# Kernel tuning notes

Hardware: AMD Instinct MI355X
Metric: run time of the kernel (lower is better)

The kernel has to match this reference:

```python
import jax, jax.numpy as jnp
import numpy as np

L = 2048
LEVEL = 4
B = 16
D = 32

# pywt 'db4' decomposition filters (dec_lo, dec_hi), hardcoded to avoid pywt dep
DB4_DEC_LO = np.array([
    -0.010597401784997278, 0.032883011666982945, 0.030841381835986965,
    -0.18703481171888114, -0.02798376941698385, 0.6308807679295904,
    0.7148465705525415, 0.23037781330885523])
DB4_DEC_HI = np.array([
    -0.23037781330885523, 0.7148465705525415, -0.6308807679295904,
    -0.02798376941698385, 0.18703481171888114, 0.030841381835986965,
    -0.032883011666982945, -0.010597401784997278])


def _wavelet_dec_filter(vec, length, level):
    # filter[j][t][(t - 2^j * i) mod L] = vec[i]  (vectorized over t, i)
    wl = len(vec)
    f = np.zeros((level, length, length), dtype=np.float32)
    t = np.arange(length)[:, None]
    i = np.arange(wl)[None, :]
    rows = np.broadcast_to(t, (length, wl))
    for j in range(level):
        idx = (t - (2 ** j) * i) % length  # (L, wl)
        f[j, rows, idx] = vec[None, :]
    return f


def setup_inputs() -> dict:
    key = jax.random.key(0)
    x = jax.random.normal(key, (B, L, D), dtype=jnp.float32)
    h = DB4_DEC_HI / np.sqrt(2.0)
    g = DB4_DEC_LO / np.sqrt(2.0)
    w_dec_filter = jnp.asarray(_wavelet_dec_filter(h, L, LEVEL))  # (J, L, L)
    v_dec_filter = jnp.asarray(_wavelet_dec_filter(g, L, LEVEL))  # (J, L, L)
    return {"x": x, "w_dec_filter": w_dec_filter, "v_dec_filter": v_dec_filter}


def reference(x, w_dec_filter, v_dec_filter):
    # MODWT: x (B, L, D) -> wavecoeff (B, D, L, level+1)
    xt = jnp.transpose(x, (0, 2, 1))  # (B, D, L)
    level = w_dec_filter.shape[0]
    v_j = xt
    vs = []
    for j in range(level):  # sequential over small fixed number of levels
        v_j = jnp.einsum('ml,bdl->bdm', v_dec_filter[j], v_j)
        vs.append(v_j)
    v = jnp.stack(vs, axis=2)  # (B, D, J, L)
    # inputs to each detail filter: [x, v_0, ..., v_{J-2}]
    v_prime = jnp.concatenate([xt[:, :, None, :], v[:, :, :-1, :]], axis=2)  # (B, D, J, L)
    w = jnp.einsum('jml,bdjl->bdjm', w_dec_filter, v_prime)  # (B, D, J, L)
    wavecoeff = jnp.concatenate([w, v[:, :, -1:, :]], axis=2)  # (B, D, J+1, L)
    return jnp.transpose(wavecoeff, (0, 1, 3, 2))  # (B, D, L, J+1)
```

## Files before the change

### kernel.cpp

```cpp
#include <hip/hip_runtime.h>

#define L_LEN 2048
#define N_LEVEL 4
#define N_B 16
#define N_D 32
#define BLOCK 256

__global__ __launch_bounds__(BLOCK) void swt_db4_kernel(const float* __restrict__ x,
                                                        float* __restrict__ out) {
    const float g[8] = {
        (float)(-0.010597401784997278 / 1.4142135623730951),
        (float)( 0.032883011666982945 / 1.4142135623730951),
        (float)( 0.030841381835986965 / 1.4142135623730951),
        (float)(-0.18703481171888114  / 1.4142135623730951),
        (float)(-0.02798376941698385  / 1.4142135623730951),
        (float)( 0.6308807679295904   / 1.4142135623730951),
        (float)( 0.7148465705525415   / 1.4142135623730951),
        (float)( 0.23037781330885523  / 1.4142135623730951)};
    const float h[8] = {
        (float)(-0.23037781330885523  / 1.4142135623730951),
        (float)( 0.7148465705525415   / 1.4142135623730951),
        (float)(-0.6308807679295904   / 1.4142135623730951),
        (float)(-0.02798376941698385  / 1.4142135623730951),
        (float)( 0.18703481171888114  / 1.4142135623730951),
        (float)( 0.030841381835986965 / 1.4142135623730951),
        (float)(-0.032883011666982945 / 1.4142135623730951),
        (float)(-0.010597401784997278 / 1.4142135623730951)};

    __shared__ float buf[2][L_LEN];

    const int bd = blockIdx.x;
    const int b  = bd >> 5;
    const int d  = bd & 31;
    const int t  = threadIdx.x;

    const float* xp = x + (size_t)b * L_LEN * N_D + d;
    float* op = out + (size_t)bd * L_LEN * 5;

    for (int l = t; l < L_LEN; l += BLOCK)
        buf[0][l] = xp[(size_t)l * N_D];
    __syncthreads();

    int cur = 0;
    #pragma unroll
    for (int j = 0; j < N_LEVEL; ++j) {
        const int dil = 1 << j;
        const float* __restrict__ src = buf[cur];
        float* __restrict__ dst = buf[cur ^ 1];

        for (int m = t; m < L_LEN; m += BLOCK) {
            float w = 0.0f, v = 0.0f;
            #pragma unroll
            for (int i = 0; i < 8; ++i) {
                const float s = src[(m - dil * i) & (L_LEN - 1)];
                w = fmaf(h[i], s, w);
                v = fmaf(g[i], s, v);
            }
            op[m * 5 + j] = w;
            if (j == N_LEVEL - 1)
                op[m * 5 + 4] = v;
            else
                dst[m] = v;
        }
        if (j != N_LEVEL - 1)
            __syncthreads();
        cur ^= 1;
    }
}

extern "C" void kernel_launch(void* const* d_in, const int* in_sizes, int n_in,
                              void* d_out, int out_size, void* d_ws, size_t ws_size,
                              hipStream_t stream) {
    const float* x = (const float*)d_in[0];
    float* out = (float*)d_out;

    swt_db4_kernel<<<N_B * N_D, BLOCK, 0, stream>>>(x, out);
}
```

Baseline: 140.4 us.

## Tile along sequence across all channels with halo recompute for coalesced loads

Each block now processes a 64-sample tile of one batch across all 32 channels, loading the input tile plus a 105-sample halo with coalesced accesses over the channel dimension. The four dilated filter levels run in shared memory, and each level shrinks the valid range by its receptive field. This replaces the strided per-channel global loads of the old layout. In exchange it recomputes halo values, roughly doubling arithmetic, and uses about 43 KB of LDS per block. Filter coefficients move to constant memory.

Result: no change. 138.8 us (-1.1%).

```diff
diff --git a/kernel.cpp b/kernel.cpp
--- a/kernel.cpp
+++ b/kernel.cpp
@@ -1,71 +1,83 @@
 #include <hip/hip_runtime.h>
 
 #define L_LEN 2048
-#define N_LEVEL 4
-#define N_B 16
-#define N_D 32
+#define N_D   32
 #define BLOCK 256
+#define TILE  64
+#define HALO  105
+#define ROWS  (TILE + HALO)
+#define LSTR  ROWS
+
+__device__ __constant__ float G_[8] = {
+    (float)(-0.010597401784997278 / 1.4142135623730951),
+    (float)( 0.032883011666982945 / 1.4142135623730951),
+    (float)( 0.030841381835986965 / 1.4142135623730951),
+    (float)(-0.18703481171888114  / 1.4142135623730951),
+    (float)(-0.02798376941698385  / 1.4142135623730951),
+    (float)( 0.6308807679295904   / 1.4142135623730951),
+    (float)( 0.7148465705525415   / 1.4142135623730951),
+    (float)( 0.23037781330885523  / 1.4142135623730951)};
+__device__ __constant__ float H_[8] = {
+    (float)(-0.23037781330885523  / 1.4142135623730951),
+    (float)( 0.7148465705525415   / 1.4142135623730951),
+    (float)(-0.6308807679295904   / 1.4142135623730951),
+    (float)(-0.02798376941698385  / 1.4142135623730951),
+    (float)( 0.18703481171888114  / 1.4142135623730951),
+    (float)( 0.030841381835986965 / 1.4142135623730951),
+    (float)(-0.032883011666982945 / 1.4142135623730951),
+    (float)(-0.010597401784997278 / 1.4142135623730951)};
+
+template <int RANGE, int PMIN, int DIL, int CH, bool VLDS, bool VOUT>
+__device__ __forceinline__ void level_pass(const float* __restrict__ src,
+                                           float* __restrict__ dst,
+                                           float* __restrict__ ob, int t) {
+    for (int idx = t; idx < N_D * RANGE; idx += BLOCK) {
+        const int d = idx / RANGE;
+        const int p = PMIN + (idx - d * RANGE);
+        const float* s = src + d * LSTR + p;
+        float w = 0.f, v = 0.f;
+#pragma unroll
+        for (int i = 0; i < 8; ++i) {
+            const float sv = s[-DIL * i];
+            w = fmaf(H_[i], sv, w);
+            v = fmaf(G_[i], sv, v);
+        }
+        if (VLDS) dst[d * LSTR + p] = v;
+        if (p >= HALO) {
+            float* o = ob + ((size_t)d * L_LEN + (p - HALO)) * 5;
+            o[CH] = w;
+            if (VOUT) o[4] = v;
+        }
+    }
+}
 
 __global__ __launch_bounds__(BLOCK) void swt_db4_kernel(const float* __restrict__ x,
                                                         float* __restrict__ out) {
-    const float g[8] = {
-        (float)(-0.010597401784997278 / 1.4142135623730951),
-        (float)( 0.032883011666982945 / 1.4142135623730951),
-        (float)( 0.030841381835986965 / 1.4142135623730951),
-        (float)(-0.18703481171888114  / 1.4142135623730951),
-        (float)(-0.02798376941698385  / 1.4142135623730951),
-        (float)( 0.6308807679295904   / 1.4142135623730951),
-        (float)( 0.7148465705525415   / 1.4142135623730951),
-        (float)( 0.23037781330885523  / 1.4142135623730951)};
-    const float h[8] = {
-        (float)(-0.23037781330885523  / 1.4142135623730951),
-        (float)( 0.7148465705525415   / 1.4142135623730951),
-        (float)(-0.6308807679295904   / 1.4142135623730951),
-        (float)(-0.02798376941698385  / 1.4142135623730951),
-        (float)( 0.18703481171888114  / 1.4142135623730951),
-        (float)( 0.030841381835986965 / 1.4142135623730951),
-        (float)(-0.032883011666982945 / 1.4142135623730951),
-        (float)(-0.010597401784997278 / 1.4142135623730951)};
+    __shared__ float bufA[N_D * LSTR];
+    __shared__ float bufB[N_D * LSTR];
 
-    __shared__ float buf[2][L_LEN];
+    const int t  = threadIdx.x;
+    const int b  = blockIdx.x >> 5;
+    const int m0 = (blockIdx.x & 31) * TILE;
 
-    const int bd = blockIdx.x;
-    const int b  = bd >> 5;
-    const int d  = bd & 31;
-    const int t  = threadIdx.x;
+    const float* xb = x + (size_t)b * (L_LEN * N_D);
+    float* ob = out + (((size_t)b * N_D) * L_LEN + m0) * 5;
 
-    const float* xp = x + (size_t)b * L_LEN * N_D + d;
-    float* op = out + (size_t)bd * L_LEN * 5;
-
-    for (int l = t; l < L_LEN; l += BLOCK)
-        buf[0][l] = xp[(size_t)l * N_D];
+    for (int idx = t; idx < N_D * ROWS; idx += BLOCK) {
+        const int p  = idx >> 5;
+        const int d  = idx & 31;
+        const int gm = (m0 + p - HALO) & (L_LEN - 1);
+        bufA[d * LSTR + p] = xb[(size_t)gm * N_D + d];
+    }
     __syncthreads();
 
-    int cur = 0;
-    #pragma unroll
-    for (int j = 0; j < N_LEVEL; ++j) {
-        const int dil = 1 << j;
-        const float* __restrict__ src = buf[cur];
-        float* __restrict__ dst = buf[cur ^ 1];
-
-        for (int m = t; m < L_LEN; m += BLOCK) {
-            float w = 0.0f, v = 0.0f;
-            #pragma unroll
-            for (int i = 0; i < 8; ++i) {
-                const float s = src[(m - dil * i) & (L_LEN - 1)];
-                w = fmaf(h[i], s, w);
-                v = fmaf(g[i], s, v);
-            }
-            op[m * 5 + j] = w;
-            if (j == N_LEVEL - 1)
-                op[m * 5 + 4] = v;
-            else
-                dst[m] = v;
-        }
-        if (j != N_LEVEL - 1)
-            __syncthreads();
-        cur ^= 1;
-    }
+    level_pass<162,   7, 1, 0, true,  false>(bufA, bufB, ob, t);
+    __syncthreads();
+    level_pass<148,  21, 2, 1, true,  false>(bufB, bufA, ob, t);
+    __syncthreads();
+    level_pass<120,  49, 4, 2, true,  false>(bufA, bufB, ob, t);
+    __syncthreads();
+    level_pass< 64, 105, 8, 3, false, true >(bufB, bufA, ob, t);
 }
 
 extern "C" void kernel_launch(void* const* d_in, const int* in_sizes, int n_in,
@@ -74,5 +86,5 @@
     const float* x = (const float*)d_in[0];
     float* out = (float*)d_out;
 
-    swt_db4_kernel<<<N_B * N_D, BLOCK, 0, stream>>>(x, out);
+    swt_db4_kernel<<<16 * 32, BLOCK, 0, stream>>>(x, out);
 }
```
